# Optimization experiments

Hardware: AMD Instinct MI355X
Metric: run time of the kernel (lower is better)

The kernel has to match this reference:

```python
import jax, jax.numpy as jnp
import numpy as np

B, T, D = 4, 2048, 1024
E, K, F = 8, 2, 4096


def setup_inputs() -> dict:
    key = jax.random.key(0)
    ks = jax.random.split(key, 6)
    s = 0.02
    return {
        "x": jax.random.normal(ks[0], (B, T, D), dtype=jnp.float32),
        "gate_w": jax.random.normal(ks[1], (D, E), dtype=jnp.float32) * s,
        "w1": jax.random.normal(ks[2], (E, D, F), dtype=jnp.float32) * s,
        "b1": jax.random.normal(ks[3], (E, F), dtype=jnp.float32) * s,
        "w2": jax.random.normal(ks[4], (E, F, D), dtype=jnp.float32) * s,
        "b2": jax.random.normal(ks[5], (E, D), dtype=jnp.float32) * s,
    }


def reference(x, gate_w, w1, b1, w2, b2):
    b, t, d = x.shape
    xf = x.reshape(-1, d)                       # [N, D]
    logits = xf @ gate_w                        # [N, E]
    topv, topi = jax.lax.top_k(logits, K)       # [N, K]
    gates = jax.nn.softmax(topv, axis=-1)       # [N, K]
    # per-token per-expert combine weight (zero for unselected experts)
    onehot = jax.nn.one_hot(topi, E, dtype=xf.dtype)       # [N, K, E]
    comb = jnp.einsum('nk,nke->ne', gates, onehot)          # [N, E]
    out = jnp.zeros_like(xf)
    for e in range(E):  # small fixed expert loop; keeps [N,F] intermediate only
        h = jax.nn.gelu(xf @ w1[e] + b1[e], approximate=False)  # [N, F]
        y = h @ w2[e] + b2[e]                                   # [N, D]
        out = out + comb[:, e:e + 1] * y
    return out.reshape(b, t, d)
```

## Files before the change

### kernel.cpp

```cpp
#include <hip/hip_runtime.h>
#include <stdint.h>
#include <stddef.h>

#define N_TOK 8192
#define DIM   1024
#define NE    8
#define NF    4096
#define TM    128
#define TN    128
#define BKK   64
#define RCAP  (N_TOK*2 + NE*TM)
#define MAXMT (N_TOK/TM)

typedef __attribute__((ext_vector_type(8))) short short8;
typedef __attribute__((ext_vector_type(4))) float f32x4;

__device__ __forceinline__ float bf2f(short s){
  unsigned u = ((unsigned)(unsigned short)s) << 16;
  return __builtin_bit_cast(float, u);
}
__device__ __forceinline__ short f2bf(float f){
  unsigned u = __builtin_bit_cast(unsigned, f);
  u += 0x7fffu + ((u >> 16) & 1u);
  return (short)(u >> 16);
}

#define GLD_LDS16(g, l) __builtin_amdgcn_global_load_lds( \
    (const __attribute__((address_space(1))) void*)(g),   \
    (__attribute__((address_space(3))) void*)(l), 16, 0, 0)

__global__ __launch_bounds__(256) void gate_kernel(
    const float* __restrict__ x, const float* __restrict__ gw,
    int* __restrict__ topi, float* __restrict__ gatev, int* __restrict__ ctrl)
{
  int t = blockIdx.x * 4 + (threadIdx.x >> 6);
  int lane = threadIdx.x & 63;
  const float* xr = x + (size_t)t * DIM;
  float p[NE];
  #pragma unroll
  for (int e = 0; e < NE; e++) p[e] = 0.f;
  for (int i = lane; i < DIM; i += 64){
    float xv = xr[i];
    const float* g = gw + i * NE;
    #pragma unroll
    for (int e = 0; e < NE; e++) p[e] += xv * g[e];
  }
  #pragma unroll
  for (int off = 32; off > 0; off >>= 1){
    #pragma unroll
    for (int e = 0; e < NE; e++) p[e] += __shfl_xor(p[e], off, 64);
  }
  if (lane == 0){
    int i1 = 0; float v1 = p[0];
    #pragma unroll
    for (int e = 1; e < NE; e++) if (p[e] > v1){ v1 = p[e]; i1 = e; }
    int i2 = -1; float v2 = -3.4e38f;
    #pragma unroll
    for (int e = 0; e < NE; e++) if (e != i1 && p[e] > v2){ v2 = p[e]; i2 = e; }
    float ex = expf(v2 - v1);
    float g2 = ex / (1.f + ex);
    float g1 = 1.f - g2;
    topi[t*2]   = i1;  topi[t*2+1]  = i2;
    gatev[t*2]  = g1;  gatev[t*2+1] = g2;
    atomicAdd(&ctrl[i1], 1);
    atomicAdd(&ctrl[i2], 1);
  }
}

__global__ void scan_kernel(int* ctrl){
  if (threadIdx.x == 0){
    int tot = 0;
    for (int e = 0; e < NE; e++){
      int c = ctrl[e];
      int cap = (c + TM - 1) & ~(TM - 1);
      ctrl[16+e] = tot; ctrl[24+e] = cap; tot += cap;
    }
  }
}

__global__ __launch_bounds__(256) void scatter_kernel(
    const int* __restrict__ topi, int* ctrl,
    int* __restrict__ rowTok, int* __restrict__ tok2row)
{
  int t = blockIdx.x * 256 + threadIdx.x;
  #pragma unroll
  for (int k = 0; k < 2; k++){
    int e = topi[t*2 + k];
    int pos = atomicAdd(&ctrl[8+e], 1);
    int r = ctrl[16+e] + pos;
    rowTok[r] = t;
    tok2row[t*2 + k] = r;
  }
}

__global__ void pad_kernel(const int* __restrict__ ctrl, int* __restrict__ rowTok){
  int e = blockIdx.x;
  int cnt = ctrl[e], cap = ctrl[24+e], off = ctrl[16+e];
  for (int i = cnt + threadIdx.x; i < cap; i += blockDim.x)
    rowTok[off + i] = N_TOK;
}

__global__ __launch_bounds__(256) void cast_x_kernel(
    const float* __restrict__ x, short* __restrict__ xb)
{
  size_t i = ((size_t)blockIdx.x * 256 + threadIdx.x) * 8;
  if (i >= (size_t)(N_TOK + 1) * DIM) return;
  short8 o;
  if (i < (size_t)N_TOK * DIM){
    #pragma unroll
    for (int j = 0; j < 8; j++) o[j] = f2bf(x[i + j]);
  } else {
    #pragma unroll
    for (int j = 0; j < 8; j++) o[j] = 0;
  }
  *(short8*)(xb + i) = o;
}

__global__ __launch_bounds__(256) void transpose_cast_kernel(
    const float* __restrict__ src, short* __restrict__ dst, int Kd, int Nd)
{
  __shared__ float Ls[64][65];
  int e = blockIdx.z;
  int k0 = blockIdx.y * 64, n0 = blockIdx.x * 64;
  const float* s = src + (size_t)e * Kd * Nd;
  short*       d = dst + (size_t)e * Kd * Nd;
  int t = threadIdx.x;
  int kr = t >> 4, nc = (t & 15) * 4;
  #pragma unroll
  for (int rr = 0; rr < 4; rr++){
    int k = rr*16 + kr;
    f32x4 v = *(const f32x4*)(s + (size_t)(k0 + k) * Nd + n0 + nc);
    Ls[k][nc+0] = v[0]; Ls[k][nc+1] = v[1];
    Ls[k][nc+2] = v[2]; Ls[k][nc+3] = v[3];
  }
  __syncthreads();
  int nr = t >> 2, kc = (t & 3) * 16;
  short o[16];
  #pragma unroll
  for (int i = 0; i < 16; i++) o[i] = f2bf(Ls[kc + i][nr]);
  short* dp = d + (size_t)(n0 + nr) * Kd + k0 + kc;
  *(short8*)(dp)     = *(short8*)&o[0];
  *(short8*)(dp + 8) = *(short8*)&o[8];
}

__global__ __launch_bounds__(256) void ffn1_kernel(
    const short* __restrict__ Xb, const short* __restrict__ W1t,
    const float* __restrict__ b1, const int* __restrict__ ctrl,
    const int* __restrict__ rowTok, short* __restrict__ H)
{
  int e = blockIdx.z, mt = blockIdx.y, nb = blockIdx.x;
  int cap = ctrl[24+e];
  if (mt * TM >= cap) return;
  int rowbase = ctrl[16+e] + mt * TM;

  __shared__ __align__(16) short As[TM][BKK];
  __shared__ __align__(16) short Bs[TN][BKK];

  int tid = threadIdx.x, w = tid >> 6, lane = tid & 63;
  int rsub = lane >> 3, ksub = lane & 7;
  int sw = (ksub ^ rsub) * 8;

  const short* ap[4];
  #pragma unroll
  for (int j = 0; j < 4; j++){
    int g = rowTok[rowbase + w*32 + j*8 + rsub];
    ap[j] = Xb + (size_t)g * DIM + sw;
  }
  const short* bbase = W1t + ((size_t)e * NF + (size_t)nb * TN) * DIM;
  const short* bp[4];
  #pragma unroll
  for (int j = 0; j < 4; j++)
    bp[j] = bbase + (size_t)((w*4 + j)*8 + rsub) * DIM + sw;

  char* AsB = (char*)As; char* BsB = (char*)Bs;
  int ml = lane & 15, q = lane >> 4;
  int wm = w & 1, wn = w >> 1;
  int mx = ml & 7;
  const short8* Ar = (const short8*)As;
  const short8* Br = (const short8*)Bs;

  f32x4 acc[4][4];
  #pragma unroll
  for (int i = 0; i < 4; i++){
    #pragma unroll
    for (int j = 0; j < 4; j++){ f32x4 z = {0.f,0.f,0.f,0.f}; acc[i][j] = z; }
  }

  for (int kb = 0; kb < DIM/BKK; kb++){
    #pragma unroll
    for (int j = 0; j < 4; j++) GLD_LDS16(ap[j] + kb*BKK, AsB + (w*4 + j)*1024);
    #pragma unroll
    for (int j = 0; j < 4; j++) GLD_LDS16(bp[j] + kb*BKK, BsB + (w*4 + j)*1024);
    __syncthreads();
    #pragma unroll
    for (int ks = 0; ks < 2; ks++){
      int c = (ks*4 + q) ^ mx;
      short8 a[4], b[4];
      #pragma unroll
      for (int mi = 0; mi < 4; mi++) a[mi] = Ar[(wm*64 + mi*16 + ml)*8 + c];
      #pragma unroll
      for (int ni = 0; ni < 4; ni++) b[ni] = Br[(wn*64 + ni*16 + ml)*8 + c];
      #pragma unroll
      for (int mi = 0; mi < 4; mi++){
        #pragma unroll
        for (int ni = 0; ni < 4; ni++)
          acc[mi][ni] = __builtin_amdgcn_mfma_f32_16x16x32_bf16(a[mi], b[ni], acc[mi][ni], 0, 0, 0);
      }
    }
    __syncthreads();
  }

  #pragma unroll
  for (int ni = 0; ni < 4; ni++){
    int f = nb*TN + wn*64 + ni*16 + ml;
    float bb = b1[e*NF + f];
    #pragma unroll
    for (int mi = 0; mi < 4; mi++){
      #pragma unroll
      for (int r = 0; r < 4; r++){
        int m = wm*64 + mi*16 + q*4 + r;
        float v = acc[mi][ni][r] + bb;
        float h = 0.5f * v * (1.f + erff(v * 0.70710678118654752f));
        H[(size_t)(rowbase + m) * NF + f] = f2bf(h);
      }
    }
  }
}

__global__ __launch_bounds__(256) void ffn2_kernel(
    const short* __restrict__ H, const short* __restrict__ W2t,
    const float* __restrict__ b2, const int* __restrict__ ctrl,
    short* __restrict__ Yp)
{
  int e = blockIdx.z, mt = blockIdx.y, nb = blockIdx.x;
  int cap = ctrl[24+e];
  if (mt * TM >= cap) return;
  int rowbase = ctrl[16+e] + mt * TM;

  __shared__ __align__(16) short As[TM][BKK];
  __shared__ __align__(16) short Bs[TN][BKK];

  int tid = threadIdx.x, w = tid >> 6, lane = tid & 63;
  int rsub = lane >> 3, ksub = lane & 7;
  int sw = (ksub ^ rsub) * 8;

  const short* ap[4];
  #pragma unroll
  for (int j = 0; j < 4; j++){
    int r = rowbase + w*32 + j*8 + rsub;
    ap[j] = H + (size_t)r * NF + sw;
  }
  const short* bbase = W2t + ((size_t)e * DIM + (size_t)nb * TN) * NF;
  const short* bp[4];
  #pragma unroll
  for (int j = 0; j < 4; j++)
    bp[j] = bbase + (size_t)((w*4 + j)*8 + rsub) * NF + sw;

  char* AsB = (char*)As; char* BsB = (char*)Bs;
  int ml = lane & 15, q = lane >> 4;
  int wm = w & 1, wn = w >> 1;
  int mx = ml & 7;
  const short8* Ar = (const short8*)As;
  const short8* Br = (const short8*)Bs;

  f32x4 acc[4][4];
  #pragma unroll
  for (int i = 0; i < 4; i++){
    #pragma unroll
    for (int j = 0; j < 4; j++){ f32x4 z = {0.f,0.f,0.f,0.f}; acc[i][j] = z; }
  }

  for (int kb = 0; kb < NF/BKK; kb++){
    #pragma unroll
    for (int j = 0; j < 4; j++) GLD_LDS16(ap[j] + kb*BKK, AsB + (w*4 + j)*1024);
    #pragma unroll
    for (int j = 0; j < 4; j++) GLD_LDS16(bp[j] + kb*BKK, BsB + (w*4 + j)*1024);
    __syncthreads();
    #pragma unroll
    for (int ks = 0; ks < 2; ks++){
      int c = (ks*4 + q) ^ mx;
      short8 a[4], b[4];
      #pragma unroll
      for (int mi = 0; mi < 4; mi++) a[mi] = Ar[(wm*64 + mi*16 + ml)*8 + c];
      #pragma unroll
      for (int ni = 0; ni < 4; ni++) b[ni] = Br[(wn*64 + ni*16 + ml)*8 + c];
      #pragma unroll
      for (int mi = 0; mi < 4; mi++){
        #pragma unroll
        for (int ni = 0; ni < 4; ni++)
          acc[mi][ni] = __builtin_amdgcn_mfma_f32_16x16x32_bf16(a[mi], b[ni], acc[mi][ni], 0, 0, 0);
      }
    }
    __syncthreads();
  }

  #pragma unroll
  for (int ni = 0; ni < 4; ni++){
    int d = nb*TN + wn*64 + ni*16 + ml;
    float bb = b2[e*DIM + d];
    #pragma unroll
    for (int mi = 0; mi < 4; mi++){
      #pragma unroll
      for (int r = 0; r < 4; r++){
        int m = wm*64 + mi*16 + q*4 + r;
        Yp[(size_t)(rowbase + m) * DIM + d] = f2bf(acc[mi][ni][r] + bb);
      }
    }
  }
}

__global__ __launch_bounds__(256) void combine_kernel(
    const short* __restrict__ Yp, const int* __restrict__ tok2row,
    const float* __restrict__ gatev, float* __restrict__ out)
{
  int idx = blockIdx.x * 256 + threadIdx.x;
  int t = idx >> 7, d8 = idx & 127;
  int r0 = tok2row[t*2], r1 = tok2row[t*2 + 1];
  float g0 = gatev[t*2], g1 = gatev[t*2 + 1];
  short8 y0 = *(const short8*)(Yp + (size_t)r0 * DIM + d8*8);
  short8 y1 = *(const short8*)(Yp + (size_t)r1 * DIM + d8*8);
  float o[8];
  #pragma unroll
  for (int j = 0; j < 8; j++) o[j] = g0 * bf2f(y0[j]) + g1 * bf2f(y1[j]);
  f32x4 v0 = {o[0], o[1], o[2], o[3]};
  f32x4 v1 = {o[4], o[5], o[6], o[7]};
  f32x4* dst = (f32x4*)(out + (size_t)t * DIM + d8*8);
  dst[0] = v0; dst[1] = v1;
}

extern "C" void kernel_launch(void* const* d_in, const int* in_sizes, int n_in,
                              void* d_out, int out_size, void* d_ws, size_t ws_size,
                              hipStream_t stream)
{
  const float* x  = (const float*)d_in[0];
  const float* gw = (const float*)d_in[1];
  const float* w1 = (const float*)d_in[2];
  const float* b1 = (const float*)d_in[3];
  const float* w2 = (const float*)d_in[4];
  const float* b2 = (const float*)d_in[5];
  float* out = (float*)d_out;

  char* ws = (char*)d_ws;
  size_t o = 0;
  int*   ctrl    = (int*)(ws + o); o += 256;
  int*   topi    = (int*)(ws + o); o += (size_t)N_TOK*2*4;
  float* gatev   = (float*)(ws + o); o += (size_t)N_TOK*2*4;
  int*   rowTok  = (int*)(ws + o); o += (size_t)RCAP*4;
  int*   tok2row = (int*)(ws + o); o += (size_t)N_TOK*2*4;
  o = (o + 255) & ~(size_t)255;
  short* Xb  = (short*)(ws + o); o += (size_t)(N_TOK + 1)*DIM*2;
  short* W1t = (short*)(ws + o); o += (size_t)NE*DIM*NF*2;
  short* W2t = (short*)(ws + o); o += (size_t)NE*NF*DIM*2;
  short* H   = (short*)(ws + o); o += (size_t)RCAP*NF*2;
  short* Yp  = (short*)(ws + o); o += (size_t)RCAP*DIM*2;
  (void)in_sizes; (void)n_in; (void)out_size;

  if (o > ws_size) return;

  hipMemsetAsync(ctrl, 0, 256, stream);
  gate_kernel<<<N_TOK/4, 256, 0, stream>>>(x, gw, topi, gatev, ctrl);
  scan_kernel<<<1, 64, 0, stream>>>(ctrl);
  scatter_kernel<<<N_TOK/256, 256, 0, stream>>>(topi, ctrl, rowTok, tok2row);
  pad_kernel<<<NE, 128, 0, stream>>>(ctrl, rowTok);
  cast_x_kernel<<<((N_TOK + 1)*DIM/8 + 255)/256, 256, 0, stream>>>(x, Xb);
  transpose_cast_kernel<<<dim3(NF/64, DIM/64, NE), 256, 0, stream>>>(w1, W1t, DIM, NF);
  transpose_cast_kernel<<<dim3(DIM/64, NF/64, NE), 256, 0, stream>>>(w2, W2t, NF, DIM);
  ffn1_kernel<<<dim3(NF/TN, MAXMT, NE), 256, 0, stream>>>(Xb, W1t, b1, ctrl, rowTok, H);
  ffn2_kernel<<<dim3(DIM/TN, MAXMT, NE), 256, 0, stream>>>(H, W2t, b2, ctrl, Yp);
  combine_kernel<<<N_TOK*(DIM/8)/256, 256, 0, stream>>>(Yp, tok2row, gatev, out);
}
```

Before: 1.128 ms.

## Rework expert GEMMs with 256x256 tiles, double-buffered LDS, XCD mapping, split-K ffn2

Both expert GEMMs move to 256x256 tiles with 512-thread blocks and a double-buffered global-to-LDS pipeline that uses explicit waitcnt, barriers and setprio. Blocks are remapped so neighbouring tiles land on the same XCD. ffn2 splits K in two and accumulates fp32 partials with atomics into a zeroed buffer, and the b2 bias add moves into the combine kernel. The aim is more data reuse per tile, overlap of loads with MFMA, and more blocks for ffn2. In exchange it adds an extra memset, fp32 atomic traffic and larger padding per expert.

```diff
diff --git a/kernel.cpp b/kernel.cpp
--- a/kernel.cpp
+++ b/kernel.cpp
@@ -6,11 +6,11 @@
 #define DIM   1024
 #define NE    8
 #define NF    4096
-#define TM    128
-#define TN    128
+#define TM    256
 #define BKK   64
 #define RCAP  (N_TOK*2 + NE*TM)
 #define MAXMT (N_TOK/TM)
+#define KS2   2
 
 typedef __attribute__((ext_vector_type(8))) short short8;
 typedef __attribute__((ext_vector_type(4))) float f32x4;
@@ -28,6 +28,17 @@
 #define GLD_LDS16(g, l) __builtin_amdgcn_global_load_lds( \
     (const __attribute__((address_space(1))) void*)(g),   \
     (__attribute__((address_space(3))) void*)(l), 16, 0, 0)
+
+__device__ __forceinline__ void xcd_map(int nx, int& xo, int& mt, int& e){
+  int h   = blockIdx.x + nx * (blockIdx.y + MAXMT * blockIdx.z);
+  int nwg = nx * MAXMT * NE;
+  int q   = nwg >> 3;
+  int wk  = (h & 7) * q + (h >> 3);
+  xo = wk % nx;
+  int r = wk / nx;
+  mt = r % MAXMT;
+  e  = r / MAXMT;
+}
 
 __global__ __launch_bounds__(256) void gate_kernel(
     const float* __restrict__ x, const float* __restrict__ gw,
@@ -143,22 +154,103 @@
   *(short8*)(dp + 8) = *(short8*)&o[8];
 }
 
-__global__ __launch_bounds__(256) void ffn1_kernel(
+
+#define FFN_DECLS                                                       \
+  __shared__ __align__(16) short As[2][256][BKK];                       \
+  __shared__ __align__(16) short Bs[2][256][BKK];                       \
+  int tid = threadIdx.x, w = tid >> 6, lane = tid & 63;                 \
+  int rsub = lane >> 3, ksub = lane & 7;                                \
+  int sw = (ksub ^ rsub) * 8;                                           \
+  char* const AsB = (char*)As; char* const BsB = (char*)Bs;             \
+  int ml = lane & 15, q = lane >> 4;                                    \
+  int wm = w >> 2, wn = w & 3;                                          \
+  int mx = ml & 7;                                                      \
+  f32x4 acc[8][4];                                                      \
+  _Pragma("unroll")                                                     \
+  for (int i = 0; i < 8; i++){                                          \
+    _Pragma("unroll")                                                   \
+    for (int j = 0; j < 4; j++){ f32x4 z = {0.f,0.f,0.f,0.f}; acc[i][j] = z; } \
+  }
+
+#define FFN_STAGE(kt, s) do{                                            \
+    char* aB_ = AsB + (s)*32768; char* bB_ = BsB + (s)*32768;           \
+    _Pragma("unroll")                                                   \
+    for (int j = 0; j < 4; j++) GLD_LDS16(ap[j] + (kt)*BKK, aB_ + (w*4+j)*1024); \
+    _Pragma("unroll")                                                   \
+    for (int j = 0; j < 4; j++) GLD_LDS16(bp[j] + (kt)*BKK, bB_ + (w*4+j)*1024); \
+  } while(0)
+
+#define FFN_PROLOGUE                                                    \
+  FFN_STAGE(0, 0);                                                      \
+  FFN_STAGE(1, 1);                                                      \
+  asm volatile("s_waitcnt vmcnt(8)" ::: "memory");                      \
+  __builtin_amdgcn_sched_barrier(0);                                    \
+  __builtin_amdgcn_s_barrier();
+
+#define LDA(mh)                                                         \
+  _Pragma("unroll")                                                     \
+  for (int mi = 0; mi < 4; mi++){                                       \
+    _Pragma("unroll")                                                   \
+    for (int ks = 0; ks < 2; ks++)                                      \
+      aq[mi][ks] = Ar[(wm*128 + (mh)*64 + mi*16 + ml)*8 + ((ks*4+q)^mx)]; \
+  }
+
+#define LDB_ALL                                                         \
+  _Pragma("unroll")                                                     \
+  for (int ni = 0; ni < 4; ni++){                                       \
+    _Pragma("unroll")                                                   \
+    for (int ks = 0; ks < 2; ks++)                                      \
+      bq[ni][ks] = Br[(wn*64 + ni*16 + ml)*8 + ((ks*4+q)^mx)];          \
+  }
+
+#define MFMA_Q(mh, nh)                                                  \
+  __builtin_amdgcn_s_barrier();                                         \
+  __builtin_amdgcn_s_setprio(1);                                        \
+  _Pragma("unroll")                                                     \
+  for (int mi = 0; mi < 4; mi++){                                       \
+    _Pragma("unroll")                                                   \
+    for (int ni = 0; ni < 2; ni++){                                     \
+      _Pragma("unroll")                                                 \
+      for (int ks = 0; ks < 2; ks++)                                    \
+        acc[(mh)*4+mi][(nh)*2+ni] = __builtin_amdgcn_mfma_f32_16x16x32_bf16( \
+            aq[mi][ks], bq[(nh)*2+ni][ks], acc[(mh)*4+mi][(nh)*2+ni], 0, 0, 0); \
+    }                                                                   \
+  }                                                                     \
+  __builtin_amdgcn_s_setprio(0);
+
+#define FFN_ITER_BODY(s)                                                \
+  const short8* Ar = (const short8*)(AsB + (s)*32768);                  \
+  const short8* Br = (const short8*)(BsB + (s)*32768);                  \
+  LDA(0); LDB_ALL;                                                      \
+  MFMA_Q(0, 0);                                                         \
+  MFMA_Q(0, 1);                                                         \
+  LDA(1);                                                               \
+  MFMA_Q(1, 0);                                                         \
+  MFMA_Q(1, 1);
+
+#define FFN_BOUNDARY(t, NT)                                             \
+  __builtin_amdgcn_s_barrier();                                         \
+  __builtin_amdgcn_sched_barrier(0);                                    \
+  if ((t) + 2 < (NT)) { FFN_STAGE((t)+2, (t)&1); }                      \
+  if ((t) + 1 < (NT)){                                                  \
+    if ((t) + 2 < (NT)) { asm volatile("s_waitcnt vmcnt(8)" ::: "memory"); } \
+    else                { asm volatile("s_waitcnt vmcnt(0)" ::: "memory"); } \
+    __builtin_amdgcn_sched_barrier(0);                                  \
+    __builtin_amdgcn_s_barrier();                                       \
+  }
+
+__global__ __launch_bounds__(512, 2) void ffn1_kernel(
     const short* __restrict__ Xb, const short* __restrict__ W1t,
     const float* __restrict__ b1, const int* __restrict__ ctrl,
     const int* __restrict__ rowTok, short* __restrict__ H)
 {
-  int e = blockIdx.z, mt = blockIdx.y, nb = blockIdx.x;
+  int e, mt, nb;
+  xcd_map(NF/256, nb, mt, e);
   int cap = ctrl[24+e];
-  if (mt * TM >= cap) return;
-  int rowbase = ctrl[16+e] + mt * TM;
-
-  __shared__ __align__(16) short As[TM][BKK];
-  __shared__ __align__(16) short Bs[TN][BKK];
-
-  int tid = threadIdx.x, w = tid >> 6, lane = tid & 63;
-  int rsub = lane >> 3, ksub = lane & 7;
-  int sw = (ksub ^ rsub) * 8;
+  if (mt * 256 >= cap) return;
+  int rowbase = ctrl[16+e] + mt * 256;
+
+  FFN_DECLS;
 
   const short* ap[4];
   #pragma unroll
@@ -166,166 +258,117 @@
     int g = rowTok[rowbase + w*32 + j*8 + rsub];
     ap[j] = Xb + (size_t)g * DIM + sw;
   }
-  const short* bbase = W1t + ((size_t)e * NF + (size_t)nb * TN) * DIM;
+  const short* bbase = W1t + ((size_t)e * NF + (size_t)nb * 256) * DIM;
   const short* bp[4];
   #pragma unroll
   for (int j = 0; j < 4; j++)
-    bp[j] = bbase + (size_t)((w*4 + j)*8 + rsub) * DIM + sw;
-
-  char* AsB = (char*)As; char* BsB = (char*)Bs;
-  int ml = lane & 15, q = lane >> 4;
-  int wm = w & 1, wn = w >> 1;
-  int mx = ml & 7;
-  const short8* Ar = (const short8*)As;
-  const short8* Br = (const short8*)Bs;
-
-  f32x4 acc[4][4];
-  #pragma unroll
-  for (int i = 0; i < 4; i++){
-    #pragma unroll
-    for (int j = 0; j < 4; j++){ f32x4 z = {0.f,0.f,0.f,0.f}; acc[i][j] = z; }
-  }
-
-  for (int kb = 0; kb < DIM/BKK; kb++){
-    #pragma unroll
-    for (int j = 0; j < 4; j++) GLD_LDS16(ap[j] + kb*BKK, AsB + (w*4 + j)*1024);
-    #pragma unroll
-    for (int j = 0; j < 4; j++) GLD_LDS16(bp[j] + kb*BKK, BsB + (w*4 + j)*1024);
-    __syncthreads();
-    #pragma unroll
-    for (int ks = 0; ks < 2; ks++){
-      int c = (ks*4 + q) ^ mx;
-      short8 a[4], b[4];
-      #pragma unroll
-      for (int mi = 0; mi < 4; mi++) a[mi] = Ar[(wm*64 + mi*16 + ml)*8 + c];
-      #pragma unroll
-      for (int ni = 0; ni < 4; ni++) b[ni] = Br[(wn*64 + ni*16 + ml)*8 + c];
+    bp[j] = bbase + (size_t)(w*32 + j*8 + rsub) * DIM + sw;
+
+  FFN_PROLOGUE;
+
+  const int NT = DIM / BKK;
+  short8 aq[4][2], bq[4][2];
+  for (int t = 0; t < NT; t++){
+    int s = t & 1;
+    { FFN_ITER_BODY(s); }
+    FFN_BOUNDARY(t, NT);
+  }
+
+  #pragma unroll
+  for (int ni = 0; ni < 4; ni++){
+    int f = nb*256 + wn*64 + ni*16 + ml;
+    float bb = b1[e*NF + f];
+    #pragma unroll
+    for (int mh = 0; mh < 2; mh++){
       #pragma unroll
       for (int mi = 0; mi < 4; mi++){
         #pragma unroll
-        for (int ni = 0; ni < 4; ni++)
-          acc[mi][ni] = __builtin_amdgcn_mfma_f32_16x16x32_bf16(a[mi], b[ni], acc[mi][ni], 0, 0, 0);
+        for (int r = 0; r < 4; r++){
+          int m = wm*128 + mh*64 + mi*16 + q*4 + r;
+          float v = acc[mh*4+mi][ni][r] + bb;
+          float h = 0.5f * v * (1.f + erff(v * 0.70710678118654752f));
+          H[(size_t)(rowbase + m) * NF + f] = f2bf(h);
+        }
       }
     }
-    __syncthreads();
-  }
-
-  #pragma unroll
-  for (int ni = 0; ni < 4; ni++){
-    int f = nb*TN + wn*64 + ni*16 + ml;
-    float bb = b1[e*NF + f];
-    #pragma unroll
-    for (int mi = 0; mi < 4; mi++){
-      #pragma unroll
-      for (int r = 0; r < 4; r++){
-        int m = wm*64 + mi*16 + q*4 + r;
-        float v = acc[mi][ni][r] + bb;
-        float h = 0.5f * v * (1.f + erff(v * 0.70710678118654752f));
-        H[(size_t)(rowbase + m) * NF + f] = f2bf(h);
-      }
-    }
-  }
-}
-
-__global__ __launch_bounds__(256) void ffn2_kernel(
+  }
+}
+
+__global__ __launch_bounds__(512, 2) void ffn2_kernel(
     const short* __restrict__ H, const short* __restrict__ W2t,
-    const float* __restrict__ b2, const int* __restrict__ ctrl,
-    short* __restrict__ Yp)
-{
-  int e = blockIdx.z, mt = blockIdx.y, nb = blockIdx.x;
+    const int* __restrict__ ctrl, float* __restrict__ Yf)
+{
+  int e, mt, xo;
+  xcd_map((DIM/256)*KS2, xo, mt, e);
+  int nb = xo & 3, kc = xo >> 2;
   int cap = ctrl[24+e];
-  if (mt * TM >= cap) return;
-  int rowbase = ctrl[16+e] + mt * TM;
-
-  __shared__ __align__(16) short As[TM][BKK];
-  __shared__ __align__(16) short Bs[TN][BKK];
-
-  int tid = threadIdx.x, w = tid >> 6, lane = tid & 63;
-  int rsub = lane >> 3, ksub = lane & 7;
-  int sw = (ksub ^ rsub) * 8;
+  if (mt * 256 >= cap) return;
+  int rowbase = ctrl[16+e] + mt * 256;
+
+  FFN_DECLS;
 
   const short* ap[4];
   #pragma unroll
   for (int j = 0; j < 4; j++){
     int r = rowbase + w*32 + j*8 + rsub;
-    ap[j] = H + (size_t)r * NF + sw;
-  }
-  const short* bbase = W2t + ((size_t)e * DIM + (size_t)nb * TN) * NF;
+    ap[j] = H + (size_t)r * NF + (size_t)kc * (NF/KS2) + sw;
+  }
+  const short* bbase = W2t + ((size_t)e * DIM + (size_t)nb * 256) * NF;
   const short* bp[4];
   #pragma unroll
   for (int j = 0; j < 4; j++)
-    bp[j] = bbase + (size_t)((w*4 + j)*8 + rsub) * NF + sw;
-
-  char* AsB = (char*)As; char* BsB = (char*)Bs;
-  int ml = lane & 15, q = lane >> 4;
-  int wm = w & 1, wn = w >> 1;
-  int mx = ml & 7;
-  const short8* Ar = (const short8*)As;
-  const short8* Br = (const short8*)Bs;
-
-  f32x4 acc[4][4];
-  #pragma unroll
-  for (int i = 0; i < 4; i++){
-    #pragma unroll
-    for (int j = 0; j < 4; j++){ f32x4 z = {0.f,0.f,0.f,0.f}; acc[i][j] = z; }
-  }
-
-  for (int kb = 0; kb < NF/BKK; kb++){
-    #pragma unroll
-    for (int j = 0; j < 4; j++) GLD_LDS16(ap[j] + kb*BKK, AsB + (w*4 + j)*1024);
-    #pragma unroll
-    for (int j = 0; j < 4; j++) GLD_LDS16(bp[j] + kb*BKK, BsB + (w*4 + j)*1024);
-    __syncthreads();
-    #pragma unroll
-    for (int ks = 0; ks < 2; ks++){
-      int c = (ks*4 + q) ^ mx;
-      short8 a[4], b[4];
-      #pragma unroll
-      for (int mi = 0; mi < 4; mi++) a[mi] = Ar[(wm*64 + mi*16 + ml)*8 + c];
-      #pragma unroll
-      for (int ni = 0; ni < 4; ni++) b[ni] = Br[(wn*64 + ni*16 + ml)*8 + c];
+    bp[j] = bbase + (size_t)(w*32 + j*8 + rsub) * NF + (size_t)kc * (NF/KS2) + sw;
+
+  FFN_PROLOGUE;
+
+  const int NT = (NF/KS2) / BKK;
+  short8 aq[4][2], bq[4][2];
+  for (int t = 0; t < NT; t++){
+    int s = t & 1;
+    { FFN_ITER_BODY(s); }
+    FFN_BOUNDARY(t, NT);
+  }
+
+  #pragma unroll
+  for (int ni = 0; ni < 4; ni++){
+    int d = nb*256 + wn*64 + ni*16 + ml;
+    #pragma unroll
+    for (int mh = 0; mh < 2; mh++){
       #pragma unroll
       for (int mi = 0; mi < 4; mi++){
         #pragma unroll
-        for (int ni = 0; ni < 4; ni++)
-          acc[mi][ni] = __builtin_amdgcn_mfma_f32_16x16x32_bf16(a[mi], b[ni], acc[mi][ni], 0, 0, 0);
+        for (int r = 0; r < 4; r++){
+          int m = wm*128 + mh*64 + mi*16 + q*4 + r;
+          atomicAdd(&Yf[(size_t)(rowbase + m) * DIM + d], acc[mh*4+mi][ni][r]);
+        }
       }
     }
-    __syncthreads();
-  }
-
-  #pragma unroll
-  for (int ni = 0; ni < 4; ni++){
-    int d = nb*TN + wn*64 + ni*16 + ml;
-    float bb = b2[e*DIM + d];
-    #pragma unroll
-    for (int mi = 0; mi < 4; mi++){
-      #pragma unroll
-      for (int r = 0; r < 4; r++){
-        int m = wm*64 + mi*16 + q*4 + r;
-        Yp[(size_t)(rowbase + m) * DIM + d] = f2bf(acc[mi][ni][r] + bb);
-      }
-    }
   }
 }
 
 __global__ __launch_bounds__(256) void combine_kernel(
-    const short* __restrict__ Yp, const int* __restrict__ tok2row,
-    const float* __restrict__ gatev, float* __restrict__ out)
+    const float* __restrict__ Yf, const int* __restrict__ tok2row,
+    const int* __restrict__ topi, const float* __restrict__ gatev,
+    const float* __restrict__ b2, float* __restrict__ out)
 {
   int idx = blockIdx.x * 256 + threadIdx.x;
   int t = idx >> 7, d8 = idx & 127;
   int r0 = tok2row[t*2], r1 = tok2row[t*2 + 1];
+  int e0 = topi[t*2],    e1 = topi[t*2 + 1];
   float g0 = gatev[t*2], g1 = gatev[t*2 + 1];
-  short8 y0 = *(const short8*)(Yp + (size_t)r0 * DIM + d8*8);
-  short8 y1 = *(const short8*)(Yp + (size_t)r1 * DIM + d8*8);
-  float o[8];
-  #pragma unroll
-  for (int j = 0; j < 8; j++) o[j] = g0 * bf2f(y0[j]) + g1 * bf2f(y1[j]);
-  f32x4 v0 = {o[0], o[1], o[2], o[3]};
-  f32x4 v1 = {o[4], o[5], o[6], o[7]};
+  const f32x4* y0 = (const f32x4*)(Yf + (size_t)r0 * DIM + d8*8);
+  const f32x4* y1 = (const f32x4*)(Yf + (size_t)r1 * DIM + d8*8);
+  const f32x4* c0 = (const f32x4*)(b2 + (size_t)e0 * DIM + d8*8);
+  const f32x4* c1 = (const f32x4*)(b2 + (size_t)e1 * DIM + d8*8);
   f32x4* dst = (f32x4*)(out + (size_t)t * DIM + d8*8);
-  dst[0] = v0; dst[1] = v1;
+  #pragma unroll
+  for (int h = 0; h < 2; h++){
+    f32x4 o;
+    #pragma unroll
+    for (int j = 0; j < 4; j++)
+      o[j] = g0 * (y0[h][j] + c0[h][j]) + g1 * (y1[h][j] + c1[h][j]);
+    dst[h] = o;
+  }
 }
 
 extern "C" void kernel_launch(void* const* d_in, const int* in_sizes, int n_in,
@@ -352,20 +395,21 @@
   short* W1t = (short*)(ws + o); o += (size_t)NE*DIM*NF*2;
   short* W2t = (short*)(ws + o); o += (size_t)NE*NF*DIM*2;
   short* H   = (short*)(ws + o); o += (size_t)RCAP*NF*2;
-  short* Yp  = (short*)(ws + o); o += (size_t)RCAP*DIM*2;
+  float* Yf  = (float*)(ws + o); o += (size_t)RCAP*DIM*4;
   (void)in_sizes; (void)n_in; (void)out_size;
 
   if (o > ws_size) return;
 
   hipMemsetAsync(ctrl, 0, 256, stream);
+  hipMemsetAsync(Yf, 0, (size_t)RCAP*DIM*4, stream);
   gate_kernel<<<N_TOK/4, 256, 0, stream>>>(x, gw, topi, gatev, ctrl);
   scan_kernel<<<1, 64, 0, stream>>>(ctrl);
   scatter_kernel<<<N_TOK/256, 256, 0, stream>>>(topi, ctrl, rowTok, tok2row);
-  pad_kernel<<<NE, 128, 0, stream>>>(ctrl, rowTok);
+  pad_kernel<<<NE, 256, 0, stream>>>(ctrl, rowTok);
   cast_x_kernel<<<((N_TOK + 1)*DIM/8 + 255)/256, 256, 0, stream>>>(x, Xb);
   transpose_cast_kernel<<<dim3(NF/64, DIM/64, NE), 256, 0, stream>>>(w1, W1t, DIM, NF);
   transpose_cast_kernel<<<dim3(DIM/64, NF/64, NE), 256, 0, stream>>>(w2, W2t, NF, DIM);
-  ffn1_kernel<<<dim3(NF/TN, MAXMT, NE), 256, 0, stream>>>(Xb, W1t, b1, ctrl, rowTok, H);
-  ffn2_kernel<<<dim3(DIM/TN, MAXMT, NE), 256, 0, stream>>>(H, W2t, b2, ctrl, Yp);
-  combine_kernel<<<N_TOK*(DIM/8)/256, 256, 0, stream>>>(Yp, tok2row, gatev, out);
-}
+  ffn1_kernel<<<dim3(NF/256, MAXMT, NE), 512, 0, stream>>>(Xb, W1t, b1, ctrl, rowTok, H);
+  ffn2_kernel<<<dim3((DIM/256)*KS2, MAXMT, NE), 512, 0, stream>>>(H, W2t, ctrl, Yf);
+  combine_kernel<<<N_TOK*(DIM/8)/256, 256, 0, stream>>>(Yf, tok2row, topi, gatev, b2, out);
+}
```

Result: slower. 1.239 ms (+9.8%).
